# Kernel tuning notes

Measured on AMD Instinct MI355X. Metric: run time of the kernel, lower is better.

Reference implementation:

```python
import jax, jax.numpy as jnp
from jax import lax
import numpy as np

B, C, H, W = 8, 256, 64, 64
STRIDE, NH = 2, 8
ED_QK, ED_V = 64, 256  # embed_dim//ratio (divisible by heads), embed_dim
HQ, WQ = H // STRIDE, W // STRIDE
L = HQ * WQ


def conv2d(x, w, b, stride=1, pad=0):
    y = lax.conv_general_dilated(x, w, (stride, stride), ((pad, pad), (pad, pad)),
                                 dimension_numbers=('NCHW', 'OIHW', 'NCHW'))
    return y + b[None, :, None, None]


def setup_inputs() -> dict:
    key = jax.random.key(0)
    ks = jax.random.split(key, 24)
    s = 0.05
    f32 = jnp.float32
    inp = {
        'qkv_pos': jax.random.normal(ks[0], (B, C, H, W), f32),
        'qkv_cha': jax.random.normal(ks[1], (B, C, H, W), f32),
        # POS branch params (standard convs)
        'Wq_pos': jax.random.normal(ks[2], (ED_QK, C, 2, 2), f32) * s,
        'bq_pos': jax.random.normal(ks[3], (ED_QK,), f32) * s,
        'Wk_pos': jax.random.normal(ks[4], (ED_QK, C, 2, 2), f32) * s,
        'bk_pos': jax.random.normal(ks[5], (ED_QK,), f32) * s,
        'Wv_pos': jax.random.normal(ks[6], (ED_V, C, 2, 2), f32) * s,
        'bv_pos': jax.random.normal(ks[7], (ED_V,), f32) * s,
        'Wo_pos': jax.random.normal(ks[8], (C, ED_V, 3, 3), f32) * s,
        'bo_pos': jax.random.normal(ks[9], (C,), f32) * s,
        'gamma_pos': jnp.full((1,), 0.5, f32),
        # CHA branch params (grouped convs, groups=C, 1 in-ch -> NH out-ch per group)
        'Wq_cha': jax.random.normal(ks[10], (C, NH, 2, 2), f32) * s,
        'bq_cha': jax.random.normal(ks[11], (C, NH), f32) * s,
        'Wk_cha': jax.random.normal(ks[12], (C, NH, 2, 2), f32) * s,
        'bk_cha': jax.random.normal(ks[13], (C, NH), f32) * s,
        'Wv_cha': jax.random.normal(ks[14], (C, NH, 2, 2), f32) * s,
        'bv_cha': jax.random.normal(ks[15], (C, NH), f32) * s,
        # grouped ConvTranspose2d (groups=C, NH in-ch per group -> 1 out-ch), k=s=2
        'Wt_cha': jax.random.normal(ks[16], (C, NH, 2, 2), f32) * s,
        'bt_cha': jax.random.normal(ks[17], (C,), f32) * s,
        'gamma_cha': jnp.full((1,), 0.5, f32),
        # fusion conv: concat -> 2C in, C out, 3x3
        'Wf': jax.random.normal(ks[18], (C, 2 * C, 3, 3), f32) * s,
        'bf': jax.random.normal(ks[19], (C,), f32) * s,
    }
    return inp


def _gproj(x, w, b):
    # grouped conv with kernel==stride==2, 1 in-ch per group -> NH out-ch per group
    xp = x.reshape(B, C, HQ, STRIDE, WQ, STRIDE)
    y = jnp.einsum('bgikjl,ghkl->bghij', xp, w) + b[None, :, :, None, None]
    # channel order c = g*NH + h (torch grouped-conv layout); torch then reshapes
    # the flat C*NH channels into (NH, C) -> same as a direct reshape here
    return y.reshape(B, NH, C, L)


def reference(qkv_pos, qkv_cha, Wq_pos, bq_pos, Wk_pos, bk_pos, Wv_pos, bv_pos,
              Wo_pos, bo_pos, gamma_pos, Wq_cha, bq_cha, Wk_cha, bk_cha,
              Wv_cha, bv_cha, Wt_cha, bt_cha, gamma_cha, Wf, bf):
    hd = ED_QK // NH
    # ---- POS (spatial) attention ----
    qp = conv2d(qkv_pos, Wq_pos, bq_pos, STRIDE).reshape(B, NH, hd, L).transpose(0, 1, 3, 2)
    kp = conv2d(qkv_pos, Wk_pos, bk_pos, STRIDE).reshape(B, NH, hd, L).transpose(0, 1, 3, 2)
    vp = conv2d(qkv_pos, Wv_pos, bv_pos, STRIDE).reshape(B, NH, ED_V // NH, L).transpose(0, 1, 3, 2)
    attn_p = jax.nn.softmax(jnp.einsum('bhqd,bhkd->bhqk', qp, kp) * (hd ** -0.5), axis=-1)
    op = jnp.einsum('bhqk,bhkd->bhqd', attn_p, vp).transpose(0, 1, 3, 2).reshape(B, ED_V, HQ, WQ)
    op = conv2d(op, Wo_pos, bo_pos, 1, 1)
    op = jax.image.resize(op, (B, C, H, W), 'bilinear')  # Upsample(align_corners=False)
    out_pos = qkv_pos + op * gamma_pos
    # ---- CHA (channel) attention ----
    qc = _gproj(qkv_cha, Wq_cha, bq_cha)  # [B,NH,C,L]
    kc = _gproj(qkv_cha, Wk_cha, bk_cha)
    vc = _gproj(qkv_cha, Wv_cha, bv_cha)
    attn_c = jax.nn.softmax(jnp.einsum('bhcl,bhdl->bhcd', qc, kc) * (L ** -0.5), axis=-1)
    oc = jnp.einsum('bhcd,bhdl->bhcl', attn_c, vc)  # [B,NH,C,L]
    # flat channel c = h*C + g; grouped ConvTranspose2d groups by c//NH -> reshape (C,NH)
    ocg = oc.reshape(B, C, NH, HQ, WQ)
    oc = jnp.einsum('bgipq,gikl->bgpkql', ocg, Wt_cha).reshape(B, C, H, W) + bt_cha[None, :, None, None]
    out_cha = qkv_cha + oc * gamma_cha
    # ---- fusion: concat (slices are full since slides=0) + 3x3 conv ----
    out = jnp.concatenate([out_pos, out_cha], axis=1)
    return conv2d(out, Wf, bf, 1, 1)
```

## Files before the change

kernel.cpp:

```cpp
#include <hip/hip_runtime.h>
#include <math.h>


typedef __attribute__((ext_vector_type(8))) short bf16x8;
typedef __attribute__((ext_vector_type(4))) float f32x4;

__device__ __forceinline__ ushort f2bf(float f) {
  union { float f; unsigned u; } v; v.f = f;
  unsigned r = (v.u + 0x7FFFu + ((v.u >> 16) & 1u)) >> 16;
  return (ushort)r;
}

template <int CIN>
__global__ __launch_bounds__(256) void k_prepack9(
    const float* __restrict__ W, ushort* __restrict__ out)
{
  const int i = blockIdx.x * 256 + threadIdx.x;
  const int t = i / (256 * CIN);
  const int r = i - t * (256 * CIN);
  const int oc = r / CIN;
  const int c = r - oc * CIN;
  out[i] = f2bf(W[((size_t)oc * CIN + c) * 9 + t]);
}

__global__ __launch_bounds__(256) void k_cast_wqkv(
    const float* __restrict__ Wq, const float* __restrict__ Wk,
    const float* __restrict__ Wv, ushort* __restrict__ out)
{
  const int i = blockIdx.x * 256 + threadIdx.x;
  const int o = i >> 10, k = i & 1023;
  float v;
  if (o < 64)       v = Wq[(size_t)o * 1024 + k];
  else if (o < 128) v = Wk[(size_t)(o - 64) * 1024 + k];
  else              v = Wv[(size_t)(o - 128) * 1024 + k];
  out[i] = f2bf(v);
}

__global__ __launch_bounds__(256) void k_zero_border(ushort* __restrict__ fused)
{
  const int t = blockIdx.x * 256 + threadIdx.x;
  const int e = t & 63;
  const int pi = (t >> 6) % 260;
  const int b = t / 16640;
  int y, x;
  if (pi < 66)       { y = 0;            x = pi; }
  else if (pi < 132) { y = 65;           x = pi - 66; }
  else if (pi < 196) { y = pi - 132 + 1; x = 0; }
  else               { y = pi - 196 + 1; x = 65; }
  uint4 z = {0u, 0u, 0u, 0u};
  *(uint4*)(fused + ((size_t)b * 4356 + y * 66 + x) * 512 + e * 8) = z;
}

__global__ __launch_bounds__(256) void k_pack_pos(
    const float* __restrict__ x, ushort* __restrict__ Ap)
{
  const int t = blockIdx.x * 256 + threadIdx.x;
  const int j4 = t & 7;
  const int i  = (t >> 3) & 31;
  const int c  = (t >> 8) & 255;
  const int b  = t >> 16;
  const float* xb = x + (((size_t)b * 256 + c) << 12) + (2 * i) * 64 + 8 * j4;
  union { float4 v[2]; float f[8]; } r0, r1;
  r0.v[0] = *(const float4*)(xb);
  r0.v[1] = *(const float4*)(xb + 4);
  r1.v[0] = *(const float4*)(xb + 64);
  r1.v[1] = *(const float4*)(xb + 68);
  #pragma unroll
  for (int jj = 0; jj < 4; ++jj) {
    const int l = i * 32 + j4 * 4 + jj;
    union { ushort u[4]; uint2 d; } pk;
    pk.u[0] = f2bf(r0.f[2 * jj]);
    pk.u[1] = f2bf(r0.f[2 * jj + 1]);
    pk.u[2] = f2bf(r1.f[2 * jj]);
    pk.u[3] = f2bf(r1.f[2 * jj + 1]);
    *(uint2*)(Ap + ((((size_t)b << 10) + l) << 10) + c * 4) = pk.d;
  }
}

__global__ __launch_bounds__(256) void k_pos_qkv_mfma(
    const ushort* __restrict__ Ap, const ushort* __restrict__ Wqkv,
    const float* __restrict__ bq, const float* __restrict__ bk,
    const float* __restrict__ bv,
    ushort* __restrict__ Qb, ushort* __restrict__ Kb, ushort* __restrict__ Vtb)
{
  const int n0 = blockIdx.x * 128, oc0 = blockIdx.y * 128, b = blockIdx.z;
  const int tid = threadIdx.x, lane = tid & 63, w = tid >> 6;
  __shared__ ushort As[128][32], Bs[128][32];
  const ushort* Abw = Wqkv + (size_t)oc0 * 1024;
  const ushort* Bb  = Ap + (((size_t)b << 10) + n0) * 1024;
  const int wr = w >> 1, wc = w & 1;
  f32x4 acc[4][4];
  #pragma unroll
  for (int mi = 0; mi < 4; ++mi)
    #pragma unroll
    for (int ni = 0; ni < 4; ++ni) {
      f32x4 z = {0.f, 0.f, 0.f, 0.f};
      acc[mi][ni] = z;
    }
  for (int kc = 0; kc < 1024; kc += 32) {
    __syncthreads();
    #pragma unroll
    for (int q = 0; q < 2; ++q) {
      int idx = w * 128 + q * 64 + lane;
      int row = idx >> 2, seg = idx & 3;
      const ushort* srcA = Abw + (size_t)row * 1024 + kc + seg * 8;
      const ushort* srcB = Bb + (size_t)row * 1024 + kc + seg * 8;
      char* dstA = (char*)&As[0][0] + w * 2048 + q * 1024;
      char* dstB = (char*)&Bs[0][0] + w * 2048 + q * 1024;
      __builtin_amdgcn_global_load_lds(
          (const __attribute__((address_space(1))) unsigned*)srcA,
          (__attribute__((address_space(3))) unsigned*)dstA, 16, 0, 0);
      __builtin_amdgcn_global_load_lds(
          (const __attribute__((address_space(1))) unsigned*)srcB,
          (__attribute__((address_space(3))) unsigned*)dstB, 16, 0, 0);
    }
    __syncthreads();
    bf16x8 af[4], bfv[4];
    #pragma unroll
    for (int mi = 0; mi < 4; ++mi)
      af[mi] = *(const bf16x8*)&As[wr * 64 + mi * 16 + (lane & 15)][(lane >> 4) * 8];
    #pragma unroll
    for (int ni = 0; ni < 4; ++ni)
      bfv[ni] = *(const bf16x8*)&Bs[wc * 64 + ni * 16 + (lane & 15)][(lane >> 4) * 8];
    #pragma unroll
    for (int mi = 0; mi < 4; ++mi)
      #pragma unroll
      for (int ni = 0; ni < 4; ++ni)
        acc[mi][ni] = __builtin_amdgcn_mfma_f32_16x16x32_bf16(
            af[mi], bfv[ni], acc[mi][ni], 0, 0, 0);
  }
  #pragma unroll
  for (int mi = 0; mi < 4; ++mi) {
    const int oc = oc0 + wr * 64 + mi * 16 + (lane >> 4) * 4;
    if (oc >= 384) continue;
    if (oc < 64) {
      const int hh = oc >> 3, e = oc & 7;
      float4 bb = *(const float4*)(bq + oc);
      #pragma unroll
      for (int ni = 0; ni < 4; ++ni) {
        const int l = n0 + wc * 64 + ni * 16 + (lane & 15);
        union { ushort u[4]; uint2 d; } pk;
        pk.u[0] = f2bf((acc[mi][ni][0] + bb.x) * 0.35355339059327373f);
        pk.u[1] = f2bf((acc[mi][ni][1] + bb.y) * 0.35355339059327373f);
        pk.u[2] = f2bf((acc[mi][ni][2] + bb.z) * 0.35355339059327373f);
        pk.u[3] = f2bf((acc[mi][ni][3] + bb.w) * 0.35355339059327373f);
        *(uint2*)(Qb + (((((size_t)b * 8 + hh) << 10) + l) << 5) + e) = pk.d;
      }
    } else if (oc < 128) {
      const int o2 = oc - 64, hh = o2 >> 3, e = o2 & 7;
      float4 bb = *(const float4*)(bk + o2);
      #pragma unroll
      for (int ni = 0; ni < 4; ++ni) {
        const int l = n0 + wc * 64 + ni * 16 + (lane & 15);
        union { ushort u[4]; uint2 d; } pk;
        pk.u[0] = f2bf(acc[mi][ni][0] + bb.x);
        pk.u[1] = f2bf(acc[mi][ni][1] + bb.y);
        pk.u[2] = f2bf(acc[mi][ni][2] + bb.z);
        pk.u[3] = f2bf(acc[mi][ni][3] + bb.w);
        *(uint2*)(Kb + (((((size_t)b * 8 + hh) << 10) + l) << 5) + e) = pk.d;
      }
    } else {
      const int o2 = oc - 128, hh = o2 >> 5, dd = o2 & 31;
      float4 bb = *(const float4*)(bv + o2);
      #pragma unroll
      for (int ni = 0; ni < 4; ++ni) {
        const int l = n0 + wc * 64 + ni * 16 + (lane & 15);
        ushort* vb = Vtb + ((((size_t)b * 8 + hh) * 32 + dd) << 10) + l;
        vb[0]      = f2bf(acc[mi][ni][0] + bb.x);
        vb[1024]   = f2bf(acc[mi][ni][1] + bb.y);
        vb[2048]   = f2bf(acc[mi][ni][2] + bb.z);
        vb[3072]   = f2bf(acc[mi][ni][3] + bb.w);
      }
    }
  }
}

__global__ __launch_bounds__(256) void k_pos_flash(
    const ushort* __restrict__ Qb, const ushort* __restrict__ Kb,
    const ushort* __restrict__ Vtb, ushort* __restrict__ op_pad)
{
  const int qt = blockIdx.x, h = blockIdx.y, b = blockIdx.z;
  const int bh = b * 8 + h;
  const int tid = threadIdx.x, lane = tid & 63, wq = tid >> 6;
  const int c = lane & 15, g = lane >> 4;
  __shared__ __align__(16) ushort Ps[4][32][72];
  const int qbase = qt * 128 + wq * 32;
  bf16x8 qf[2];
  #pragma unroll
  for (int nt = 0; nt < 2; ++nt)
    qf[nt] = *(const bf16x8*)(Qb + (((size_t)bh << 10) + qbase + nt * 16 + c) * 32 + g * 8);
  f32x4 o[2][2];
  #pragma unroll
  for (int mt = 0; mt < 2; ++mt)
    #pragma unroll
    for (int nt = 0; nt < 2; ++nt) {
      f32x4 z = {0.f, 0.f, 0.f, 0.f};
      o[mt][nt] = z;
    }
  float m[2] = {-1e30f, -1e30f}, l[2] = {0.f, 0.f};
  const ushort* Kbh = Kb + ((size_t)bh << 15);
  const ushort* Vbh = Vtb + ((size_t)bh << 15);

  for (int kt = 0; kt < 16; ++kt) {
    const int kb0 = kt * 64;
    bf16x8 kf[4];
    #pragma unroll
    for (int mt = 0; mt < 4; ++mt)
      kf[mt] = *(const bf16x8*)(Kbh + (size_t)(kb0 + mt * 16 + c) * 32 + g * 8);
    f32x4 s[4][2];
    #pragma unroll
    for (int mt = 0; mt < 4; ++mt)
      #pragma unroll
      for (int nt = 0; nt < 2; ++nt) {
        f32x4 z = {0.f, 0.f, 0.f, 0.f};
        s[mt][nt] = __builtin_amdgcn_mfma_f32_16x16x32_bf16(kf[mt], qf[nt], z, 0, 0, 0);
      }
    #pragma unroll
    for (int nt = 0; nt < 2; ++nt) {
      float tmax = -1e30f;
      #pragma unroll
      for (int mt = 0; mt < 4; ++mt)
        #pragma unroll
        for (int r = 0; r < 4; ++r)
          tmax = fmaxf(tmax, s[mt][nt][r]);
      tmax = fmaxf(tmax, __shfl_xor(tmax, 16, 64));
      tmax = fmaxf(tmax, __shfl_xor(tmax, 32, 64));
      const float mn = fmaxf(m[nt], tmax);
      const float alpha = __expf(m[nt] - mn);
      m[nt] = mn;
      float rs = 0.f;
      #pragma unroll
      for (int mt = 0; mt < 4; ++mt) {
        union { ushort u[4]; uint2 d; } pk;
        #pragma unroll
        for (int r = 0; r < 4; ++r) {
          float p = __expf(s[mt][nt][r] - mn);
          rs += p;
          pk.u[r] = f2bf(p);
        }
        *(uint2*)&Ps[wq][nt * 16 + c][mt * 16 + g * 4] = pk.d;
      }
      rs += __shfl_xor(rs, 16, 64);
      rs += __shfl_xor(rs, 32, 64);
      l[nt] = l[nt] * alpha + rs;
      #pragma unroll
      for (int mt = 0; mt < 2; ++mt)
        #pragma unroll
        for (int r = 0; r < 4; ++r)
          o[mt][nt][r] *= alpha;
    }
    #pragma unroll
    for (int kc = 0; kc < 2; ++kc) {
      bf16x8 vf[2], pf[2];
      #pragma unroll
      for (int mt = 0; mt < 2; ++mt)
        vf[mt] = *(const bf16x8*)(Vbh + (size_t)(mt * 16 + c) * 1024 + kb0 + kc * 32 + g * 8);
      #pragma unroll
      for (int nt = 0; nt < 2; ++nt)
        pf[nt] = *(const bf16x8*)&Ps[wq][nt * 16 + c][kc * 32 + g * 8];
      #pragma unroll
      for (int mt = 0; mt < 2; ++mt)
        #pragma unroll
        for (int nt = 0; nt < 2; ++nt)
          o[mt][nt] = __builtin_amdgcn_mfma_f32_16x16x32_bf16(vf[mt], pf[nt], o[mt][nt], 0, 0, 0);
    }
  }
  #pragma unroll
  for (int nt = 0; nt < 2; ++nt) {
    const float linv = 1.f / l[nt];
    const int q = qbase + nt * 16 + c;
    const int y = q >> 5, x = q & 31;
    ushort* dst = op_pad + ((size_t)b * 1156 + (y + 1) * 34 + (x + 1)) * 256 + h * 32;
    #pragma unroll
    for (int mt = 0; mt < 2; ++mt) {
      union { ushort u[4]; uint2 d; } pk;
      #pragma unroll
      for (int r = 0; r < 4; ++r)
        pk.u[r] = f2bf(o[mt][nt][r] * linv);
      *(uint2*)(dst + mt * 16 + g * 4) = pk.d;
    }
  }
}

template <int CIN, int S, int PW, int OUT_NHWC>
__global__ __launch_bounds__(256) void k_conv9_mfma(
    const ushort* __restrict__ in, const ushort* __restrict__ W9,
    const float* __restrict__ bias, float* __restrict__ out)
{
  const int n0 = blockIdx.x * 128, oc0 = blockIdx.y * 128, b = blockIdx.z;
  const int tid = threadIdx.x, lane = tid & 63, w = tid >> 6;
  __shared__ ushort As[128][32], Bs[128][32];
  const int wr = w >> 1, wc = w & 1;
  f32x4 acc[4][4];
  #pragma unroll
  for (int mi = 0; mi < 4; ++mi)
    #pragma unroll
    for (int ni = 0; ni < 4; ++ni) {
      f32x4 z = {0.f, 0.f, 0.f, 0.f};
      acc[mi][ni] = z;
    }
  int rowq[2], segq[2], basep[2];
  #pragma unroll
  for (int q = 0; q < 2; ++q) {
    int idx = w * 128 + q * 64 + lane;
    rowq[q] = idx >> 2;
    segq[q] = (idx & 3) * 8;
    int n = n0 + rowq[q];
    int y = n / S, x = n % S;
    basep[q] = y * PW + x;
  }
  const ushort* inb = in + (size_t)b * (PW * PW) * CIN;

  for (int t = 0; t < 9; ++t) {
    const int offp = (t / 3) * PW + (t % 3);
    const ushort* wt = W9 + (size_t)t * 256 * CIN;
    for (int kc = 0; kc < CIN; kc += 32) {
      __syncthreads();
      #pragma unroll
      for (int q = 0; q < 2; ++q) {
        const ushort* srcA = wt + (size_t)(oc0 + rowq[q]) * CIN + kc + segq[q];
        const ushort* srcB = inb + (size_t)(basep[q] + offp) * CIN + kc + segq[q];
        char* dstA = (char*)&As[0][0] + w * 2048 + q * 1024;
        char* dstB = (char*)&Bs[0][0] + w * 2048 + q * 1024;
        __builtin_amdgcn_global_load_lds(
            (const __attribute__((address_space(1))) unsigned*)srcA,
            (__attribute__((address_space(3))) unsigned*)dstA, 16, 0, 0);
        __builtin_amdgcn_global_load_lds(
            (const __attribute__((address_space(1))) unsigned*)srcB,
            (__attribute__((address_space(3))) unsigned*)dstB, 16, 0, 0);
      }
      __syncthreads();
      bf16x8 af[4], bfv[4];
      #pragma unroll
      for (int mi = 0; mi < 4; ++mi)
        af[mi] = *(const bf16x8*)&As[wr * 64 + mi * 16 + (lane & 15)][(lane >> 4) * 8];
      #pragma unroll
      for (int ni = 0; ni < 4; ++ni)
        bfv[ni] = *(const bf16x8*)&Bs[wc * 64 + ni * 16 + (lane & 15)][(lane >> 4) * 8];
      #pragma unroll
      for (int mi = 0; mi < 4; ++mi)
        #pragma unroll
        for (int ni = 0; ni < 4; ++ni)
          acc[mi][ni] = __builtin_amdgcn_mfma_f32_16x16x32_bf16(
              af[mi], bfv[ni], acc[mi][ni], 0, 0, 0);
    }
  }
  if (OUT_NHWC) {
    float* outb = out + (size_t)b * (S * S) * 256;
    #pragma unroll
    for (int mi = 0; mi < 4; ++mi) {
      const int oc = oc0 + wr * 64 + mi * 16 + (lane >> 4) * 4;
      float4 bb = *(const float4*)(bias + oc);
      #pragma unroll
      for (int ni = 0; ni < 4; ++ni) {
        const int n = n0 + wc * 64 + ni * 16 + (lane & 15);
        float4 v;
        v.x = acc[mi][ni][0] + bb.x;
        v.y = acc[mi][ni][1] + bb.y;
        v.z = acc[mi][ni][2] + bb.z;
        v.w = acc[mi][ni][3] + bb.w;
        *(float4*)(outb + (size_t)n * 256 + oc) = v;
      }
    }
  } else {
    float* outb = out + (size_t)b * 256 * (S * S);
    #pragma unroll
    for (int mi = 0; mi < 4; ++mi) {
      #pragma unroll
      for (int r = 0; r < 4; ++r) {
        int oc = oc0 + wr * 64 + mi * 16 + (lane >> 4) * 4 + r;
        float bb = bias[oc];
        #pragma unroll
        for (int ni = 0; ni < 4; ++ni) {
          int n = n0 + wc * 64 + ni * 16 + (lane & 15);
          outb[(size_t)oc * (S * S) + n] = acc[mi][ni][r] + bb;
        }
      }
    }
  }
}

#define STAGE_CONV(s_, bi_)                                                    \
  {                                                                            \
    const int t_ = (s_) >> 3, kc_ = ((s_) & 7) << 6;                           \
    const ushort* wt_ = W9 + t_ * 131072 + kc_;                                \
    const ushort* ib_ = inb + ((t_ / 3) * 66 + (t_ % 3)) * 512 + kc_;          \
    _Pragma("unroll")                                                          \
    for (int q_ = 0; q_ < 2; ++q_) {                                           \
      __builtin_amdgcn_global_load_lds(                                        \
          (const __attribute__((address_space(1))) unsigned*)(wt_ + aInv[q_]), \
          (__attribute__((address_space(3))) unsigned*)                        \
              ((char*)lds + (bi_) * 16384 + (w * 16 + q_ * 8) * 128),          \
          16, 0, 0);                                                           \
    }                                                                          \
    _Pragma("unroll")                                                          \
    for (int q_ = 0; q_ < 4; ++q_) {                                           \
      __builtin_amdgcn_global_load_lds(                                        \
          (const __attribute__((address_space(1))) unsigned*)(ib_ + bInv[q_]), \
          (__attribute__((address_space(3))) unsigned*)                        \
              ((char*)lds + 49152 + (bi_) * 32768 + (w * 32 + q_ * 8) * 128),  \
          16, 0, 0);                                                           \
    }                                                                          \
  }

#define READ_FRAGS(rb_, AF_, BF_)                                              \
  {                                                                            \
    const ushort* As_ = lds + (rb_) * 8192 + (wm * 64 + c) * 64;               \
    const ushort* Bs_ = lds + 24576 + (rb_) * 16384 + (wn * 64 + c) * 64;      \
    _Pragma("unroll")                                                          \
    for (int mi_ = 0; mi_ < 4; ++mi_) {                                        \
      AF_[mi_][0] = *(const bf16x8*)(As_ + mi_ * 1024 + okh0);                 \
      AF_[mi_][1] = *(const bf16x8*)(As_ + mi_ * 1024 + okh1);                 \
    }                                                                          \
    _Pragma("unroll")                                                          \
    for (int ni_ = 0; ni_ < 4; ++ni_) {                                        \
      BF_[ni_][0] = *(const bf16x8*)(Bs_ + ni_ * 1024 + okh0);                 \
      BF_[ni_][1] = *(const bf16x8*)(Bs_ + ni_ * 1024 + okh1);                 \
    }                                                                          \
  }

#define MFMA_SET(AF_, BF_)                                                     \
  {                                                                            \
    __builtin_amdgcn_s_setprio(1);                                             \
    _Pragma("unroll")                                                          \
    for (int mi_ = 0; mi_ < 4; ++mi_)                                          \
      _Pragma("unroll")                                                        \
      for (int ni_ = 0; ni_ < 4; ++ni_) {                                      \
        acc[mi_][ni_] = __builtin_amdgcn_mfma_f32_16x16x32_bf16(               \
            AF_[mi_][0], BF_[ni_][0], acc[mi_][ni_], 0, 0, 0);                 \
        acc[mi_][ni_] = __builtin_amdgcn_mfma_f32_16x16x32_bf16(               \
            AF_[mi_][1], BF_[ni_][1], acc[mi_][ni_], 0, 0, 0);                 \
      }                                                                        \
    __builtin_amdgcn_s_setprio(0);                                             \
  }

#define PHASE_END(vm_)                                                         \
  {                                                                            \
    asm volatile("s_waitcnt lgkmcnt(0)" ::: "memory");                         \
    asm volatile("s_waitcnt vmcnt(" #vm_ ")" ::: "memory");                    \
    __builtin_amdgcn_sched_barrier(0);                                         \
    __builtin_amdgcn_s_barrier();                                              \
  }

#define LOADS_FIRST() __builtin_amdgcn_sched_barrier(0)

__global__ __launch_bounds__(512, 2) void k_conv9_pipe(
    const ushort* __restrict__ in, const ushort* __restrict__ W9,
    const float* __restrict__ bias, float* __restrict__ out)
{
  const int n0 = blockIdx.x * 256, oc0 = blockIdx.y * 128, b = blockIdx.z;
  const int tid = threadIdx.x, lane = tid & 63, w = tid >> 6;
  const int wm = w >> 2, wn = w & 3;
  const int g = lane >> 4, c = lane & 15;
  __shared__ __align__(16) ushort lds[73728];
  const ushort* inb = in + (size_t)b * 4356 * 512;

  const int l8 = lane >> 3, lx = lane & 7;
  int aInv[2], bInv[4];
  #pragma unroll
  for (int q = 0; q < 2; ++q) {
    const int row = w * 16 + q * 8 + l8;
    const int cx = (((lx << 4) ^ ((row & 7) << 4)) >> 1);
    aInv[q] = (oc0 + row) * 512 + cx;
  }
  #pragma unroll
  for (int q = 0; q < 4; ++q) {
    const int row = w * 32 + q * 8 + l8;
    const int n = n0 + row;
    const int y = n >> 6, x = n & 63;
    const int cx = (((lx << 4) ^ ((row & 7) << 4)) >> 1);
    bInv[q] = (y * 66 + x) * 512 + cx;
  }

  const int sx = (c & 7) << 3;
  const int okh0 = (g * 8) ^ sx;
  const int okh1 = (32 + g * 8) ^ sx;

  f32x4 acc[4][4];
  #pragma unroll
  for (int mi = 0; mi < 4; ++mi)
    #pragma unroll
    for (int ni = 0; ni < 4; ++ni) {
      f32x4 z = {0.f, 0.f, 0.f, 0.f};
      acc[mi][ni] = z;
    }

  bf16x8 afE[4][2], bfE[4][2], afO[4][2], bfO[4][2];

  STAGE_CONV(0, 0);
  STAGE_CONV(1, 1);
  STAGE_CONV(2, 2);
  asm volatile("s_waitcnt vmcnt(12)" ::: "memory");
  __builtin_amdgcn_sched_barrier(0);
  __builtin_amdgcn_s_barrier();
  READ_FRAGS(0, afE, bfE);
  PHASE_END(6);

  int rb = 1;
  for (int p = 0; p < 68; p += 2) {
    READ_FRAGS(rb, afO, bfO);
    { int sb = rb + 2; if (sb >= 3) sb -= 3; STAGE_CONV(p + 3, sb); }
    LOADS_FIRST();
    MFMA_SET(afE, bfE);
    PHASE_END(6);
    ++rb; if (rb == 3) rb = 0;
    READ_FRAGS(rb, afE, bfE);
    { int sb = rb + 2; if (sb >= 3) sb -= 3; STAGE_CONV(p + 4, sb); }
    LOADS_FIRST();
    MFMA_SET(afO, bfO);
    PHASE_END(6);
    ++rb; if (rb == 3) rb = 0;
  }
  READ_FRAGS(rb, afO, bfO);
  { int sb = rb + 2; if (sb >= 3) sb -= 3; STAGE_CONV(71, sb); }
  LOADS_FIRST();
  MFMA_SET(afE, bfE);
  PHASE_END(6);
  ++rb; if (rb == 3) rb = 0;
  READ_FRAGS(rb, afE, bfE);
  LOADS_FIRST();
  MFMA_SET(afO, bfO);
  PHASE_END(0);
  ++rb; if (rb == 3) rb = 0;
  READ_FRAGS(rb, afO, bfO);
  LOADS_FIRST();
  MFMA_SET(afE, bfE);
  asm volatile("s_waitcnt lgkmcnt(0)" ::: "memory");
  __builtin_amdgcn_sched_barrier(0);
  __builtin_amdgcn_s_barrier();
  MFMA_SET(afO, bfO);

  float* outb = out + (size_t)b * 1048576;
  #pragma unroll
  for (int mi = 0; mi < 4; ++mi) {
    const int oc = oc0 + wm * 64 + mi * 16 + g * 4;
    float4 bb = *(const float4*)(bias + oc);
    #pragma unroll
    for (int ni = 0; ni < 4; ++ni) {
      const int n = n0 + wn * 64 + ni * 16 + c;
      outb[(size_t)(oc + 0) * 4096 + n] = acc[mi][ni][0] + bb.x;
      outb[(size_t)(oc + 1) * 4096 + n] = acc[mi][ni][1] + bb.y;
      outb[(size_t)(oc + 2) * 4096 + n] = acc[mi][ni][2] + bb.z;
      outb[(size_t)(oc + 3) * 4096 + n] = acc[mi][ni][3] + bb.w;
    }
  }
}

__global__ __launch_bounds__(256) void k_upsample_nhwc(
    const float* __restrict__ xpos, const float* __restrict__ opc,
    const float* __restrict__ gamma, ushort* __restrict__ fused)
{
  const int t = blockIdx.x * 256 + threadIdx.x;
  const int c = (t & 63) * 4;
  const int pix = (t >> 6) & 4095;
  const int b = t >> 18;
  const int y = pix >> 6, xx = pix & 63;
  const int my = y >> 1;
  const int y0 = (y & 1) ? my : my - 1;
  const float fy = (y & 1) ? 0.25f : 0.75f;
  const int mx = xx >> 1;
  const int x0 = (xx & 1) ? mx : mx - 1;
  const float fx = (xx & 1) ? 0.25f : 0.75f;
  const int y0c = max(y0, 0), y1c = min(y0 + 1, 31);
  const int x0c = max(x0, 0), x1c = min(x0 + 1, 31);
  const float* base = opc + (size_t)b * 1024 * 256 + c;
  float4 v00 = *(const float4*)(base + (size_t)(y0c * 32 + x0c) * 256);
  float4 v01 = *(const float4*)(base + (size_t)(y0c * 32 + x1c) * 256);
  float4 v10 = *(const float4*)(base + (size_t)(y1c * 32 + x0c) * 256);
  float4 v11 = *(const float4*)(base + (size_t)(y1c * 32 + x1c) * 256);
  const float w00 = (1.f - fy) * (1.f - fx), w01 = (1.f - fy) * fx;
  const float w10 = fy * (1.f - fx), w11 = fy * fx;
  const float g = gamma[0];
  const float* xr = xpos + ((size_t)b * 256 + c) * 4096 + pix;
  union { ushort u[4]; uint2 q; } o;
  o.u[0] = f2bf(xr[0]          + g * (w00 * v00.x + w01 * v01.x + w10 * v10.x + w11 * v11.x));
  o.u[1] = f2bf(xr[4096]       + g * (w00 * v00.y + w01 * v01.y + w10 * v10.y + w11 * v11.y));
  o.u[2] = f2bf(xr[2 * 4096]   + g * (w00 * v00.z + w01 * v01.z + w10 * v10.z + w11 * v11.z));
  o.u[3] = f2bf(xr[3 * 4096]   + g * (w00 * v00.w + w01 * v01.w + w10 * v10.w + w11 * v11.w));
  *(uint2*)(fused + ((size_t)b * 4356 + (y + 1) * 66 + (xx + 1)) * 512 + c) = o.q;
}

__global__ __launch_bounds__(256) void k_cha_proj(
    const float* __restrict__ x,
    const float* __restrict__ Wq, const float* __restrict__ bq,
    const float* __restrict__ Wk, const float* __restrict__ bk,
    const float* __restrict__ Wv, const float* __restrict__ bv,
    ushort* __restrict__ Qc, ushort* __restrict__ Kc, ushort* __restrict__ Vt)
{
  const int t = blockIdx.x * 256 + threadIdx.x;
  const int bl = t >> 16;
  const int g  = (t >> 8) & 255;
  const int lq = t & 255;
  const int i = lq >> 3, j4 = (lq & 7) << 2;
  const float* xb = x + (((size_t)bl * 256 + g) << 12) + (2 * i) * 64 + 2 * j4;
  union { float4 v[2]; float f[8]; } xr0, xr1;
  xr0.v[0] = *(const float4*)(xb);
  xr0.v[1] = *(const float4*)(xb + 4);
  xr1.v[0] = *(const float4*)(xb + 64);
  xr1.v[1] = *(const float4*)(xb + 68);
  const int bhl = bl * 8 + (g >> 5);
  const int c2b = (g & 31) * 8;
  const int l0 = i * 32 + j4;
  #pragma unroll
  for (int h = 0; h < 8; ++h) {
    float4 w4 = *(const float4*)(Wq + g * 32 + h * 4);
    float bb = bq[g * 8 + h];
    union { ushort u[4]; uint2 q; } o;
    #pragma unroll
    for (int jj = 0; jj < 4; ++jj) {
      float v = xr0.f[2 * jj] * w4.x + xr0.f[2 * jj + 1] * w4.y
              + xr1.f[2 * jj] * w4.z + xr1.f[2 * jj + 1] * w4.w + bb;
      o.u[jj] = f2bf(v * 0.03125f);
    }
    *(uint2*)(Qc + (((size_t)bhl * 256 + c2b + h) << 10) + l0) = o.q;
  }
  #pragma unroll
  for (int h = 0; h < 8; ++h) {
    float4 w4 = *(const float4*)(Wk + g * 32 + h * 4);
    float bb = bk[g * 8 + h];
    union { ushort u[4]; uint2 q; } o;
    #pragma unroll
    for (int jj = 0; jj < 4; ++jj) {
      float v = xr0.f[2 * jj] * w4.x + xr0.f[2 * jj + 1] * w4.y
              + xr1.f[2 * jj] * w4.z + xr1.f[2 * jj + 1] * w4.w + bb;
      o.u[jj] = f2bf(v);
    }
    *(uint2*)(Kc + (((size_t)bhl * 256 + c2b + h) << 10) + l0) = o.q;
  }
  ushort vo[4][8];
  #pragma unroll
  for (int h = 0; h < 8; ++h) {
    float4 w4 = *(const float4*)(Wv + g * 32 + h * 4);
    float bb = bv[g * 8 + h];
    #pragma unroll
    for (int jj = 0; jj < 4; ++jj) {
      float v = xr0.f[2 * jj] * w4.x + xr0.f[2 * jj + 1] * w4.y
              + xr1.f[2 * jj] * w4.z + xr1.f[2 * jj + 1] * w4.w + bb;
      vo[jj][h] = f2bf(v);
    }
  }
  #pragma unroll
  for (int jj = 0; jj < 4; ++jj)
    *(uint4*)(Vt + ((size_t)bhl << 18) + (size_t)(l0 + jj) * 256 + c2b) =
        *(uint4*)&vo[jj][0];
}

__global__ __launch_bounds__(256) void k_cha_scores_mfma(
    const ushort* __restrict__ Qc, const ushort* __restrict__ Kc,
    float* __restrict__ S)
{
  const int c0 = blockIdx.x * 128, d0 = blockIdx.y * 128, bhl = blockIdx.z;
  const int tid = threadIdx.x, lane = tid & 63, w = tid >> 6;
  __shared__ ushort As[128][32], Bs[128][32];
  const ushort* Ab = Qc + ((size_t)bhl * 256 + c0) * 1024;
  const ushort* Bb = Kc + ((size_t)bhl * 256 + d0) * 1024;
  const int wr = w >> 1, wc = w & 1;
  f32x4 acc[4][4];
  #pragma unroll
  for (int mi = 0; mi < 4; ++mi)
    #pragma unroll
    for (int ni = 0; ni < 4; ++ni) {
      f32x4 z = {0.f, 0.f, 0.f, 0.f};
      acc[mi][ni] = z;
    }
  for (int kc = 0; kc < 1024; kc += 32) {
    __syncthreads();
    #pragma unroll
    for (int q = 0; q < 2; ++q) {
      int idx = w * 128 + q * 64 + lane;
      int row = idx >> 2, seg = idx & 3;
      const ushort* srcA = Ab + (size_t)row * 1024 + kc + seg * 8;
      const ushort* srcB = Bb + (size_t)row * 1024 + kc + seg * 8;
      char* dstA = (char*)&As[0][0] + w * 2048 + q * 1024;
      char* dstB = (char*)&Bs[0][0] + w * 2048 + q * 1024;
      __builtin_amdgcn_global_load_lds(
          (const __attribute__((address_space(1))) unsigned*)srcA,
          (__attribute__((address_space(3))) unsigned*)dstA, 16, 0, 0);
      __builtin_amdgcn_global_load_lds(
          (const __attribute__((address_space(1))) unsigned*)srcB,
          (__attribute__((address_space(3))) unsigned*)dstB, 16, 0, 0);
    }
    __syncthreads();
    bf16x8 af[4], bfv[4];
    #pragma unroll
    for (int mi = 0; mi < 4; ++mi)
      af[mi] = *(const bf16x8*)&As[wr * 64 + mi * 16 + (lane & 15)][(lane >> 4) * 8];
    #pragma unroll
    for (int ni = 0; ni < 4; ++ni)
      bfv[ni] = *(const bf16x8*)&Bs[wc * 64 + ni * 16 + (lane & 15)][(lane >> 4) * 8];
    #pragma unroll
    for (int mi = 0; mi < 4; ++mi)
      #pragma unroll
      for (int ni = 0; ni < 4; ++ni)
        acc[mi][ni] = __builtin_amdgcn_mfma_f32_16x16x32_bf16(
            af[mi], bfv[ni], acc[mi][ni], 0, 0, 0);
  }
  float* Sb = S + ((size_t)bhl << 16);
  #pragma unroll
  for (int mi = 0; mi < 4; ++mi)
    #pragma unroll
    for (int r = 0; r < 4; ++r) {
      int c = c0 + wr * 64 + mi * 16 + (lane >> 4) * 4 + r;
      #pragma unroll
      for (int ni = 0; ni < 4; ++ni) {
        int d = d0 + wc * 64 + ni * 16 + (lane & 15);
        Sb[(size_t)c * 256 + d] = acc[mi][ni][r];
      }
    }
}

__global__ __launch_bounds__(256) void k_softmax_p(
    const float* __restrict__ S, ushort* __restrict__ P)
{
  const int row = blockIdx.x * 4 + (threadIdx.x >> 6);
  const int lane = threadIdx.x & 63;
  const float* r = S + (size_t)row * 256;
  float4 v = *(const float4*)(r + lane * 4);
  float m = fmaxf(fmaxf(v.x, v.y), fmaxf(v.z, v.w));
  #pragma unroll
  for (int off = 32; off; off >>= 1) m = fmaxf(m, __shfl_xor(m, off, 64));
  v.x = __expf(v.x - m); v.y = __expf(v.y - m);
  v.z = __expf(v.z - m); v.w = __expf(v.w - m);
  float s = v.x + v.y + v.z + v.w;
  #pragma unroll
  for (int off = 32; off; off >>= 1) s += __shfl_xor(s, off, 64);
  const float inv = 1.f / s;
  union { ushort u[4]; uint2 q; } o;
  o.u[0] = f2bf(v.x * inv); o.u[1] = f2bf(v.y * inv);
  o.u[2] = f2bf(v.z * inv); o.u[3] = f2bf(v.w * inv);
  *(uint2*)(P + (size_t)row * 256 + lane * 4) = o.q;
}

__global__ __launch_bounds__(256) void k_cha_pv(
    const ushort* __restrict__ P, const ushort* __restrict__ Vt,
    const float* __restrict__ x,
    const float* __restrict__ Wt, const float* __restrict__ bt,
    const float* __restrict__ gamma, ushort* __restrict__ fused, int bbase)
{
  const int n0 = blockIdx.x * 128, c0 = blockIdx.y * 128, bhl = blockIdx.z;
  const int b = bbase + (bhl >> 3), h = bhl & 7;
  const int tid = threadIdx.x, lane = tid & 63, w = tid >> 6;
  __shared__ ushort As[128][32], Bs[128][32];
  __shared__ ushort Ot[512][16];
  __shared__ float wt_s[16][32];
  __shared__ float bt_s[16];
  const int gp_base = h * 32 + (c0 >> 3);
  {
    int e = tid;
    wt_s[e >> 5][e & 31] = Wt[(size_t)gp_base * 32 + e];
    e += 256;
    wt_s[e >> 5][e & 31] = Wt[(size_t)gp_base * 32 + e];
    if (tid < 16) bt_s[tid] = bt[gp_base + tid];
  }
  const ushort* Ab = P + (((size_t)bhl << 8) + c0) * 256;
  const ushort* Bb = Vt + ((size_t)bhl << 18) + (size_t)n0 * 256;
  const int wr = w >> 1, wc = w & 1;
  f32x4 acc[4][4];
  #pragma unroll
  for (int mi = 0; mi < 4; ++mi)
    #pragma unroll
    for (int ni = 0; ni < 4; ++ni) {
      f32x4 z = {0.f, 0.f, 0.f, 0.f};
      acc[mi][ni] = z;
    }
  for (int kc = 0; kc < 256; kc += 32) {
    __syncthreads();
    #pragma unroll
    for (int q = 0; q < 2; ++q) {
      int idx = w * 128 + q * 64 + lane;
      int row = idx >> 2, seg = idx & 3;
      const ushort* srcA = Ab + (size_t)row * 256 + kc + seg * 8;
      const ushort* srcB = Bb + (size_t)row * 256 + kc + seg * 8;
      char* dstA = (char*)&As[0][0] + w * 2048 + q * 1024;
      char* dstB = (char*)&Bs[0][0] + w * 2048 + q * 1024;
      __builtin_amdgcn_global_load_lds(
          (const __attribute__((address_space(1))) unsigned*)srcA,
          (__attribute__((address_space(3))) unsigned*)dstA, 16, 0, 0);
      __builtin_amdgcn_global_load_lds(
          (const __attribute__((address_space(1))) unsigned*)srcB,
          (__attribute__((address_space(3))) unsigned*)dstB, 16, 0, 0);
    }
    __syncthreads();
    bf16x8 af[4], bfv[4];
    #pragma unroll
    for (int mi = 0; mi < 4; ++mi)
      af[mi] = *(const bf16x8*)&As[wr * 64 + mi * 16 + (lane & 15)][(lane >> 4) * 8];
    #pragma unroll
    for (int ni = 0; ni < 4; ++ni)
      bfv[ni] = *(const bf16x8*)&Bs[wc * 64 + ni * 16 + (lane & 15)][(lane >> 4) * 8];
    #pragma unroll
    for (int mi = 0; mi < 4; ++mi)
      #pragma unroll
      for (int ni = 0; ni < 4; ++ni)
        acc[mi][ni] = __builtin_amdgcn_mfma_f32_16x16x32_bf16(
            af[mi], bfv[ni], acc[mi][ni], 0, 0, 0);
  }
  const float gm = gamma[0];
  const int col = lane & 15, q = lane >> 4;
  #pragma unroll
  for (int mi = 0; mi < 4; ++mi) {
    const int gloc = wr * 8 + mi * 2 + (q >> 1);
    const int gp = gp_base + gloc;
    const float btv = bt_s[gloc];
    #pragma unroll
    for (int ni = 0; ni < 4; ++ni) {
      float pa[4] = {0.f, 0.f, 0.f, 0.f};
      #pragma unroll
      for (int r = 0; r < 4; ++r) {
        const int i2 = (q & 1) * 4 + r;
        const float a = acc[mi][ni][r];
        pa[0] += a * wt_s[gloc][i2 * 4 + 0];
        pa[1] += a * wt_s[gloc][i2 * 4 + 1];
        pa[2] += a * wt_s[gloc][i2 * 4 + 2];
        pa[3] += a * wt_s[gloc][i2 * 4 + 3];
      }
      float v0 = pa[0] + __shfl_xor(pa[0], 16, 64);
      float v1 = pa[1] + __shfl_xor(pa[1], 16, 64);
      float v2 = pa[2] + __shfl_xor(pa[2], 16, 64);
      float v3 = pa[3] + __shfl_xor(pa[3], 16, 64);
      const int lloc = wc * 64 + ni * 16 + col;
      const int l = n0 + lloc;
      const int p = l >> 5, j = l & 31;
      const int y = 2 * p + (q & 1);
      const float va = (q & 1) ? v2 : v0;
      const float vb = (q & 1) ? v3 : v1;
      const float* xc = x + (((size_t)b * 256 + gp) << 12) + (y << 6) + 2 * j;
      const int lp = (lloc << 2) + (q & 1) * 2;
      Ot[lp][gloc]     = f2bf(xc[0] + gm * (va + btv));
      Ot[lp + 1][gloc] = f2bf(xc[1] + gm * (vb + btv));
    }
  }
  __syncthreads();
  #pragma unroll
  for (int pp2 = 0; pp2 < 2; ++pp2) {
    const int pixl = tid * 2 + pp2;
    const int lloc = pixl >> 2;
    const int l = n0 + lloc;
    const int p = l >> 5, j = l & 31;
    const int yy = 2 * p + ((pixl >> 1) & 1) + 1;
    const int xx = 2 * j + (pixl & 1) + 1;
    const uint4* src = (const uint4*)&Ot[pixl][0];
    uint4* dst = (uint4*)(fused + ((size_t)b * 4356 + yy * 66 + xx) * 512 + 256 + gp_base);
    dst[0] = src[0];
    dst[1] = src[1];
  }
}

extern "C" void kernel_launch(void* const* d_in, const int* in_sizes, int n_in,
                              void* d_out, int out_size, void* d_ws, size_t ws_size,
                              hipStream_t stream)
{
  (void)in_sizes; (void)n_in; (void)out_size; (void)ws_size;
  const float* qkv_pos   = (const float*)d_in[0];
  const float* qkv_cha   = (const float*)d_in[1];
  const float* Wq_pos    = (const float*)d_in[2];
  const float* bq_pos    = (const float*)d_in[3];
  const float* Wk_pos    = (const float*)d_in[4];
  const float* bk_pos    = (const float*)d_in[5];
  const float* Wv_pos    = (const float*)d_in[6];
  const float* bv_pos    = (const float*)d_in[7];
  const float* Wo_pos    = (const float*)d_in[8];
  const float* bo_pos    = (const float*)d_in[9];
  const float* gamma_pos = (const float*)d_in[10];
  const float* Wq_cha    = (const float*)d_in[11];
  const float* bq_cha    = (const float*)d_in[12];
  const float* Wk_cha    = (const float*)d_in[13];
  const float* bk_cha    = (const float*)d_in[14];
  const float* Wv_cha    = (const float*)d_in[15];
  const float* bv_cha    = (const float*)d_in[16];
  const float* Wt_cha    = (const float*)d_in[17];
  const float* bt_cha    = (const float*)d_in[18];
  const float* gamma_cha = (const float*)d_in[19];
  const float* Wf        = (const float*)d_in[20];
  const float* bf        = (const float*)d_in[21];
  float* out = (float*)d_out;

  float* ws = (float*)d_ws;
  ushort* Wpf9    = (ushort*)ws;
  ushort* Wpo9    = (ushort*)(ws + 589824);
  ushort* Qb      = (ushort*)(ws + 884736);
  ushort* Kb      = (ushort*)(ws + 1933312);
  ushort* Vtb     = (ushort*)(ws + 2981888);
  ushort* op_pad  = (ushort*)(ws + 4030464);
  float*  op_conv = ws + 5214208;
  ushort* Ap      = (ushort*)(ws + 7311360);
  ushort* qcb     = (ushort*)(ws + 884736);
  ushort* kcb     = (ushort*)(ws + 5079040);
  ushort* vcT     = (ushort*)(ws + 9273344);
  float*  attn_c  = ws + 13467648;
  ushort* Pb      = (ushort*)(ws + 15564800);
  ushort* fusedb  = (ushort*)(ws + 16613376);
  ushort* Wqkvp   = (ushort*)(ws + 25534464);

  hipMemsetAsync(op_pad, 0, (size_t)2367488 * 2, stream);
  hipMemsetAsync(Qb, 0, (size_t)2097152 * 2, stream);
  k_zero_border<<<dim3(520), 256, 0, stream>>>(fusedb);
  k_prepack9<512><<<dim3(4608), 256, 0, stream>>>(Wf, Wpf9);
  k_prepack9<256><<<dim3(2304), 256, 0, stream>>>(Wo_pos, Wpo9);
  k_cast_wqkv<<<dim3(1536), 256, 0, stream>>>(Wq_pos, Wk_pos, Wv_pos, Wqkvp);
  k_pack_pos<<<dim3(2048), 256, 0, stream>>>(qkv_pos, Ap);
  k_pos_qkv_mfma<<<dim3(8, 3, 8), 256, 0, stream>>>(Ap, Wqkvp,
      bq_pos, bk_pos, bv_pos, Qb, Kb, Vtb);
  k_pos_flash<<<dim3(8, 8, 8), 256, 0, stream>>>(Qb, Kb, Vtb, op_pad);
  k_conv9_mfma<256, 32, 34, 1><<<dim3(8, 2, 8), 256, 0, stream>>>(
      op_pad, Wpo9, bo_pos, op_conv);
  k_upsample_nhwc<<<dim3(8192), 256, 0, stream>>>(qkv_pos, op_conv, gamma_pos, fusedb);
  for (int half = 0; half < 2; ++half) {
    const float* xh = qkv_cha + (size_t)half * 4 * 256 * 4096;
    k_cha_proj<<<dim3(1024), 256, 0, stream>>>(xh, Wq_cha, bq_cha,
        Wk_cha, bk_cha, Wv_cha, bv_cha, qcb, kcb, vcT);
    k_cha_scores_mfma<<<dim3(2, 2, 32), 256, 0, stream>>>(qcb, kcb, attn_c);
    k_softmax_p<<<dim3(2048), 256, 0, stream>>>(attn_c, Pb);
    k_cha_pv<<<dim3(8, 2, 32), 256, 0, stream>>>(Pb, vcT, qkv_cha,
        Wt_cha, bt_cha, gamma_cha, fusedb, half * 4);
  }
  k_conv9_pipe<<<dim3(16, 2, 8), 512, 0, stream>>>(fusedb, Wpf9, bf, out);
}
```

Baseline: 538.8 us.

## Merge setup launches, halve N-tiles for small convs and scores, drop sched barriers

The memsets, border zeroing and three weight-prepack kernels are merged into two launches, and op_pad now has only its border zeroed instead of the whole buffer. The position output conv and the channel score GEMM use narrower N tiles (64 instead of 128), which doubles the grid to fill more CUs. The sched_barrier calls that forced loads first in the pipelined fusion conv are removed, leaving instruction ordering to the compiler. In exchange, each block gets less data reuse, and the scheduler may interleave loads and MFMAs differently than before.

```diff
diff --git a/kernel.cpp b/kernel.cpp
--- a/kernel.cpp
+++ b/kernel.cpp
@@ -11,44 +11,67 @@
   return (ushort)r;
 }
 
-template <int CIN>
-__global__ __launch_bounds__(256) void k_prepack9(
-    const float* __restrict__ W, ushort* __restrict__ out)
+__global__ __launch_bounds__(256) void k_prep_all(
+    const float* __restrict__ Wf, const float* __restrict__ Wo,
+    const float* __restrict__ Wq, const float* __restrict__ Wk,
+    const float* __restrict__ Wv,
+    ushort* __restrict__ Wpf9, ushort* __restrict__ Wpo9,
+    ushort* __restrict__ Wqkvp)
 {
   const int i = blockIdx.x * 256 + threadIdx.x;
-  const int t = i / (256 * CIN);
-  const int r = i - t * (256 * CIN);
-  const int oc = r / CIN;
-  const int c = r - oc * CIN;
-  out[i] = f2bf(W[((size_t)oc * CIN + c) * 9 + t]);
-}
-
-__global__ __launch_bounds__(256) void k_cast_wqkv(
-    const float* __restrict__ Wq, const float* __restrict__ Wk,
-    const float* __restrict__ Wv, ushort* __restrict__ out)
-{
-  const int i = blockIdx.x * 256 + threadIdx.x;
-  const int o = i >> 10, k = i & 1023;
-  float v;
-  if (o < 64)       v = Wq[(size_t)o * 1024 + k];
-  else if (o < 128) v = Wk[(size_t)(o - 64) * 1024 + k];
-  else              v = Wv[(size_t)(o - 128) * 1024 + k];
-  out[i] = f2bf(v);
-}
-
-__global__ __launch_bounds__(256) void k_zero_border(ushort* __restrict__ fused)
+  if (i < 1179648) {
+    const int t = i / 131072;
+    const int r = i - t * 131072;
+    const int oc = r >> 9, c = r & 511;
+    Wpf9[i] = f2bf(Wf[((size_t)oc * 512 + c) * 9 + t]);
+  } else if (i < 1179648 + 589824) {
+    const int j = i - 1179648;
+    const int t = j / 65536;
+    const int r = j - t * 65536;
+    const int oc = r >> 8, c = r & 255;
+    Wpo9[j] = f2bf(Wo[((size_t)oc * 256 + c) * 9 + t]);
+  } else {
+    const int j = i - 1769472;
+    const int o = j >> 10, k = j & 1023;
+    float v;
+    if (o < 64)       v = Wq[(size_t)o * 1024 + k];
+    else if (o < 128) v = Wk[(size_t)(o - 64) * 1024 + k];
+    else              v = Wv[(size_t)(o - 128) * 1024 + k];
+    Wqkvp[j] = f2bf(v);
+  }
+}
+
+__global__ __launch_bounds__(256) void k_zero_init(
+    ushort* __restrict__ fused, ushort* __restrict__ op_pad,
+    ushort* __restrict__ Qb)
 {
   const int t = blockIdx.x * 256 + threadIdx.x;
-  const int e = t & 63;
-  const int pi = (t >> 6) % 260;
-  const int b = t / 16640;
-  int y, x;
-  if (pi < 66)       { y = 0;            x = pi; }
-  else if (pi < 132) { y = 65;           x = pi - 66; }
-  else if (pi < 196) { y = pi - 132 + 1; x = 0; }
-  else               { y = pi - 196 + 1; x = 65; }
   uint4 z = {0u, 0u, 0u, 0u};
-  *(uint4*)(fused + ((size_t)b * 4356 + y * 66 + x) * 512 + e * 8) = z;
+  if (t < 133120) {
+    const int e = t & 63;
+    const int pi = (t >> 6) % 260;
+    const int b = t / 16640;
+    int y, x;
+    if (pi < 66)       { y = 0;            x = pi; }
+    else if (pi < 132) { y = 65;           x = pi - 66; }
+    else if (pi < 196) { y = pi - 132 + 1; x = 0; }
+    else               { y = pi - 196 + 1; x = 65; }
+    *(uint4*)(fused + ((size_t)b * 4356 + y * 66 + x) * 512 + e * 8) = z;
+  } else if (t < 133120 + 33792) {
+    const int j = t - 133120;
+    const int e = j & 31;
+    const int pi = (j >> 5) % 132;
+    const int b = j / 4224;
+    int y, x;
+    if (pi < 34)       { y = 0;            x = pi; }
+    else if (pi < 68)  { y = 33;           x = pi - 34; }
+    else if (pi < 100) { y = pi - 68 + 1;  x = 0; }
+    else               { y = pi - 100 + 1; x = 33; }
+    *(uint4*)(op_pad + ((size_t)b * 1156 + y * 34 + x) * 256 + e * 8) = z;
+  } else {
+    const int j = t - 166912;
+    *(uint4*)(Qb + (size_t)j * 8) = z;
+  }
 }
 
 __global__ __launch_bounds__(256) void k_pack_pos(
@@ -282,30 +305,39 @@
   }
 }
 
-template <int CIN, int S, int PW, int OUT_NHWC>
+template <int CIN, int S, int PW, int OUT_NHWC, int BN>
 __global__ __launch_bounds__(256) void k_conv9_mfma(
     const ushort* __restrict__ in, const ushort* __restrict__ W9,
     const float* __restrict__ bias, float* __restrict__ out)
 {
-  const int n0 = blockIdx.x * 128, oc0 = blockIdx.y * 128, b = blockIdx.z;
+  constexpr int BQ = BN / 64;
+  constexpr int NI = BN / 32;
+  const int n0 = blockIdx.x * BN, oc0 = blockIdx.y * 128, b = blockIdx.z;
   const int tid = threadIdx.x, lane = tid & 63, w = tid >> 6;
-  __shared__ ushort As[128][32], Bs[128][32];
+  __shared__ ushort As[128][32], Bs[BN][32];
   const int wr = w >> 1, wc = w & 1;
-  f32x4 acc[4][4];
+  f32x4 acc[4][NI];
   #pragma unroll
   for (int mi = 0; mi < 4; ++mi)
     #pragma unroll
-    for (int ni = 0; ni < 4; ++ni) {
+    for (int ni = 0; ni < NI; ++ni) {
       f32x4 z = {0.f, 0.f, 0.f, 0.f};
       acc[mi][ni] = z;
     }
-  int rowq[2], segq[2], basep[2];
+  int rowqA[2], segqA[2];
   #pragma unroll
   for (int q = 0; q < 2; ++q) {
     int idx = w * 128 + q * 64 + lane;
-    rowq[q] = idx >> 2;
-    segq[q] = (idx & 3) * 8;
-    int n = n0 + rowq[q];
+    rowqA[q] = idx >> 2;
+    segqA[q] = (idx & 3) * 8;
+  }
+  int rowqB[BQ], segqB[BQ], basep[BQ];
+  #pragma unroll
+  for (int q = 0; q < BQ; ++q) {
+    int idx = (BQ == 2) ? (w * 128 + q * 64 + lane) : tid;
+    rowqB[q] = idx >> 2;
+    segqB[q] = (idx & 3) * 8;
+    int n = n0 + rowqB[q];
     int y = n / S, x = n % S;
     basep[q] = y * PW + x;
   }
@@ -318,29 +350,32 @@
       __syncthreads();
       #pragma unroll
       for (int q = 0; q < 2; ++q) {
-        const ushort* srcA = wt + (size_t)(oc0 + rowq[q]) * CIN + kc + segq[q];
-        const ushort* srcB = inb + (size_t)(basep[q] + offp) * CIN + kc + segq[q];
+        const ushort* srcA = wt + (size_t)(oc0 + rowqA[q]) * CIN + kc + segqA[q];
         char* dstA = (char*)&As[0][0] + w * 2048 + q * 1024;
-        char* dstB = (char*)&Bs[0][0] + w * 2048 + q * 1024;
         __builtin_amdgcn_global_load_lds(
             (const __attribute__((address_space(1))) unsigned*)srcA,
             (__attribute__((address_space(3))) unsigned*)dstA, 16, 0, 0);
+      }
+      #pragma unroll
+      for (int q = 0; q < BQ; ++q) {
+        const ushort* srcB = inb + (size_t)(basep[q] + offp) * CIN + kc + segqB[q];
+        char* dstB = (char*)&Bs[0][0] + w * (BQ * 1024) + q * 1024;
         __builtin_amdgcn_global_load_lds(
             (const __attribute__((address_space(1))) unsigned*)srcB,
             (__attribute__((address_space(3))) unsigned*)dstB, 16, 0, 0);
       }
       __syncthreads();
-      bf16x8 af[4], bfv[4];
+      bf16x8 af[4], bfv[NI];
       #pragma unroll
       for (int mi = 0; mi < 4; ++mi)
         af[mi] = *(const bf16x8*)&As[wr * 64 + mi * 16 + (lane & 15)][(lane >> 4) * 8];
       #pragma unroll
-      for (int ni = 0; ni < 4; ++ni)
-        bfv[ni] = *(const bf16x8*)&Bs[wc * 64 + ni * 16 + (lane & 15)][(lane >> 4) * 8];
+      for (int ni = 0; ni < NI; ++ni)
+        bfv[ni] = *(const bf16x8*)&Bs[wc * (BN / 2) + ni * 16 + (lane & 15)][(lane >> 4) * 8];
       #pragma unroll
       for (int mi = 0; mi < 4; ++mi)
         #pragma unroll
-        for (int ni = 0; ni < 4; ++ni)
+        for (int ni = 0; ni < NI; ++ni)
           acc[mi][ni] = __builtin_amdgcn_mfma_f32_16x16x32_bf16(
               af[mi], bfv[ni], acc[mi][ni], 0, 0, 0);
     }
@@ -352,8 +387,8 @@
       const int oc = oc0 + wr * 64 + mi * 16 + (lane >> 4) * 4;
       float4 bb = *(const float4*)(bias + oc);
       #pragma unroll
-      for (int ni = 0; ni < 4; ++ni) {
-        const int n = n0 + wc * 64 + ni * 16 + (lane & 15);
+      for (int ni = 0; ni < NI; ++ni) {
+        const int n = n0 + wc * (BN / 2) + ni * 16 + (lane & 15);
         float4 v;
         v.x = acc[mi][ni][0] + bb.x;
         v.y = acc[mi][ni][1] + bb.y;
@@ -371,8 +406,8 @@
         int oc = oc0 + wr * 64 + mi * 16 + (lane >> 4) * 4 + r;
         float bb = bias[oc];
         #pragma unroll
-        for (int ni = 0; ni < 4; ++ni) {
-          int n = n0 + wc * 64 + ni * 16 + (lane & 15);
+        for (int ni = 0; ni < NI; ++ni) {
+          int n = n0 + wc * (BN / 2) + ni * 16 + (lane & 15);
           outb[(size_t)oc * (S * S) + n] = acc[mi][ni][r] + bb;
         }
       }
@@ -442,8 +477,6 @@
     __builtin_amdgcn_s_barrier();                                              \
   }
 
-#define LOADS_FIRST() __builtin_amdgcn_sched_barrier(0)
-
 __global__ __launch_bounds__(512, 2) void k_conv9_pipe(
     const ushort* __restrict__ in, const ushort* __restrict__ W9,
     const float* __restrict__ bias, float* __restrict__ out)
@@ -500,30 +533,25 @@
   for (int p = 0; p < 68; p += 2) {
     READ_FRAGS(rb, afO, bfO);
     { int sb = rb + 2; if (sb >= 3) sb -= 3; STAGE_CONV(p + 3, sb); }
-    LOADS_FIRST();
     MFMA_SET(afE, bfE);
     PHASE_END(6);
     ++rb; if (rb == 3) rb = 0;
     READ_FRAGS(rb, afE, bfE);
     { int sb = rb + 2; if (sb >= 3) sb -= 3; STAGE_CONV(p + 4, sb); }
-    LOADS_FIRST();
     MFMA_SET(afO, bfO);
     PHASE_END(6);
     ++rb; if (rb == 3) rb = 0;
   }
   READ_FRAGS(rb, afO, bfO);
   { int sb = rb + 2; if (sb >= 3) sb -= 3; STAGE_CONV(71, sb); }
-  LOADS_FIRST();
   MFMA_SET(afE, bfE);
   PHASE_END(6);
   ++rb; if (rb == 3) rb = 0;
   READ_FRAGS(rb, afE, bfE);
-  LOADS_FIRST();
   MFMA_SET(afO, bfO);
   PHASE_END(0);
   ++rb; if (rb == 3) rb = 0;
   READ_FRAGS(rb, afO, bfO);
-  LOADS_FIRST();
   MFMA_SET(afE, bfE);
   asm volatile("s_waitcnt lgkmcnt(0)" ::: "memory");
   __builtin_amdgcn_sched_barrier(0);
@@ -649,17 +677,17 @@
     const ushort* __restrict__ Qc, const ushort* __restrict__ Kc,
     float* __restrict__ S)
 {
-  const int c0 = blockIdx.x * 128, d0 = blockIdx.y * 128, bhl = blockIdx.z;
+  const int c0 = blockIdx.x * 128, d0 = blockIdx.y * 64, bhl = blockIdx.z;
   const int tid = threadIdx.x, lane = tid & 63, w = tid >> 6;
-  __shared__ ushort As[128][32], Bs[128][32];
+  __shared__ ushort As[128][32], Bs[64][32];
   const ushort* Ab = Qc + ((size_t)bhl * 256 + c0) * 1024;
   const ushort* Bb = Kc + ((size_t)bhl * 256 + d0) * 1024;
   const int wr = w >> 1, wc = w & 1;
-  f32x4 acc[4][4];
+  f32x4 acc[4][2];
   #pragma unroll
   for (int mi = 0; mi < 4; ++mi)
     #pragma unroll
-    for (int ni = 0; ni < 4; ++ni) {
+    for (int ni = 0; ni < 2; ++ni) {
       f32x4 z = {0.f, 0.f, 0.f, 0.f};
       acc[mi][ni] = z;
     }
@@ -670,28 +698,32 @@
       int idx = w * 128 + q * 64 + lane;
       int row = idx >> 2, seg = idx & 3;
       const ushort* srcA = Ab + (size_t)row * 1024 + kc + seg * 8;
-      const ushort* srcB = Bb + (size_t)row * 1024 + kc + seg * 8;
       char* dstA = (char*)&As[0][0] + w * 2048 + q * 1024;
-      char* dstB = (char*)&Bs[0][0] + w * 2048 + q * 1024;
       __builtin_amdgcn_global_load_lds(
           (const __attribute__((address_space(1))) unsigned*)srcA,
           (__attribute__((address_space(3))) unsigned*)dstA, 16, 0, 0);
+    }
+    {
+      int idx = tid;
+      int row = idx >> 2, seg = idx & 3;
+      const ushort* srcB = Bb + (size_t)row * 1024 + kc + seg * 8;
+      char* dstB = (char*)&Bs[0][0] + w * 1024;
       __builtin_amdgcn_global_load_lds(
           (const __attribute__((address_space(1))) unsigned*)srcB,
           (__attribute__((address_space(3))) unsigned*)dstB, 16, 0, 0);
     }
     __syncthreads();
-    bf16x8 af[4], bfv[4];
+    bf16x8 af[4], bfv[2];
     #pragma unroll
     for (int mi = 0; mi < 4; ++mi)
       af[mi] = *(const bf16x8*)&As[wr * 64 + mi * 16 + (lane & 15)][(lane >> 4) * 8];
     #pragma unroll
-    for (int ni = 0; ni < 4; ++ni)
-      bfv[ni] = *(const bf16x8*)&Bs[wc * 64 + ni * 16 + (lane & 15)][(lane >> 4) * 8];
+    for (int ni = 0; ni < 2; ++ni)
+      bfv[ni] = *(const bf16x8*)&Bs[wc * 32 + ni * 16 + (lane & 15)][(lane >> 4) * 8];
     #pragma unroll
     for (int mi = 0; mi < 4; ++mi)
       #pragma unroll
-      for (int ni = 0; ni < 4; ++ni)
+      for (int ni = 0; ni < 2; ++ni)
         acc[mi][ni] = __builtin_amdgcn_mfma_f32_16x16x32_bf16(
             af[mi], bfv[ni], acc[mi][ni], 0, 0, 0);
   }
@@ -702,8 +734,8 @@
     for (int r = 0; r < 4; ++r) {
       int c = c0 + wr * 64 + mi * 16 + (lane >> 4) * 4 + r;
       #pragma unroll
-      for (int ni = 0; ni < 4; ++ni) {
-        int d = d0 + wc * 64 + ni * 16 + (lane & 15);
+      for (int ni = 0; ni < 2; ++ni) {
+        int d = d0 + wc * 32 + ni * 16 + (lane & 15);
         Sb[(size_t)c * 256 + d] = acc[mi][ni][r];
       }
     }
@@ -892,24 +924,21 @@
   ushort* fusedb  = (ushort*)(ws + 16613376);
   ushort* Wqkvp   = (ushort*)(ws + 25534464);
 
-  hipMemsetAsync(op_pad, 0, (size_t)2367488 * 2, stream);
-  hipMemsetAsync(Qb, 0, (size_t)2097152 * 2, stream);
-  k_zero_border<<<dim3(520), 256, 0, stream>>>(fusedb);
-  k_prepack9<512><<<dim3(4608), 256, 0, stream>>>(Wf, Wpf9);
-  k_prepack9<256><<<dim3(2304), 256, 0, stream>>>(Wo_pos, Wpo9);
-  k_cast_wqkv<<<dim3(1536), 256, 0, stream>>>(Wq_pos, Wk_pos, Wv_pos, Wqkvp);
+  k_zero_init<<<dim3(1676), 256, 0, stream>>>(fusedb, op_pad, Qb);
+  k_prep_all<<<dim3(8448), 256, 0, stream>>>(Wf, Wo_pos, Wq_pos, Wk_pos,
+      Wv_pos, Wpf9, Wpo9, Wqkvp);
   k_pack_pos<<<dim3(2048), 256, 0, stream>>>(qkv_pos, Ap);
   k_pos_qkv_mfma<<<dim3(8, 3, 8), 256, 0, stream>>>(Ap, Wqkvp,
       bq_pos, bk_pos, bv_pos, Qb, Kb, Vtb);
   k_pos_flash<<<dim3(8, 8, 8), 256, 0, stream>>>(Qb, Kb, Vtb, op_pad);
-  k_conv9_mfma<256, 32, 34, 1><<<dim3(8, 2, 8), 256, 0, stream>>>(
+  k_conv9_mfma<256, 32, 34, 1, 64><<<dim3(16, 2, 8), 256, 0, stream>>>(
       op_pad, Wpo9, bo_pos, op_conv);
   k_upsample_nhwc<<<dim3(8192), 256, 0, stream>>>(qkv_pos, op_conv, gamma_pos, fusedb);
   for (int half = 0; half < 2; ++half) {
     const float* xh = qkv_cha + (size_t)half * 4 * 256 * 4096;
     k_cha_proj<<<dim3(1024), 256, 0, stream>>>(xh, Wq_cha, bq_cha,
         Wk_cha, bk_cha, Wv_cha, bv_cha, qcb, kcb, vcT);
-    k_cha_scores_mfma<<<dim3(2, 2, 32), 256, 0, stream>>>(qcb, kcb, attn_c);
+    k_cha_scores_mfma<<<dim3(2, 4, 32), 256, 0, stream>>>(qcb, kcb, attn_c);
     k_softmax_p<<<dim3(2048), 256, 0, stream>>>(attn_c, Pb);
     k_cha_pv<<<dim3(8, 2, 32), 256, 0, stream>>>(Pb, vcT, qkv_cha,
         Wt_cha, bt_cha, gamma_cha, fusedb, half * 4);
```

After: 520.0 us. -3.5%, faster.
